# Optimization experiments

Hardware: AMD Instinct MI355X
Metric: run time of the kernel (lower is better)

Reference implementation:

```python
import jax, jax.numpy as jnp
import numpy as np

DIM = 2048
H = 16
HD = 128
S = 2640          # frame_seq_len(22*40=880) * num_frame_per_block(3)
CACHE = 5280      # 6 cached frames
MAXPOS = 8192
EPS = 1e-6


def rmsnorm(x, g, eps=EPS):
    return x * jax.lax.rsqrt(jnp.mean(x * x, axis=-1, keepdims=True) + eps) * g


def apply_rope_interleaved(x, cos, sin):
    # x: [s, H, HD]; cos/sin: [s, HD//2]; is_neox=False -> adjacent pairs
    x1 = x[..., 0::2]
    x2 = x[..., 1::2]
    c = cos[:, None, :]
    s_ = sin[:, None, :]
    o1 = x1 * c - x2 * s_
    o2 = x2 * c + x1 * s_
    return jnp.stack([o1, o2], axis=-1).reshape(x.shape)


def setup_inputs() -> dict:
    key = jax.random.key(0)
    ks = jax.random.split(key, 10)
    w_scale = DIM ** -0.5
    x = jax.random.normal(ks[0], (1, S, DIM), dtype=jnp.float32)
    # cos_sin_cache: [max_pos, HD] = [cos(HD//2) | sin(HD//2)], real rope values
    inv_freq = 1.0 / (10000.0 ** (np.arange(0, HD, 2, dtype=np.float32) / HD))
    t = np.arange(MAXPOS, dtype=np.float32)
    ang = np.outer(t, inv_freq)  # [MAXPOS, HD//2]
    freqs = jnp.asarray(np.concatenate([np.cos(ang), np.sin(ang)], axis=1), dtype=jnp.float32)
    k_cache = jax.random.normal(ks[1], (CACHE, H, HD), dtype=jnp.float32)
    v_cache = jax.random.normal(ks[2], (CACHE, H, HD), dtype=jnp.float32)
    Wq = jax.random.normal(ks[3], (DIM, DIM), dtype=jnp.float32) * w_scale
    Wk = jax.random.normal(ks[4], (DIM, DIM), dtype=jnp.float32) * w_scale
    Wv = jax.random.normal(ks[5], (DIM, DIM), dtype=jnp.float32) * w_scale
    Wo = jax.random.normal(ks[6], (DIM, DIM), dtype=jnp.float32) * w_scale
    bq = jnp.zeros((DIM,), jnp.float32)
    bk = jnp.zeros((DIM,), jnp.float32)
    bv = jnp.zeros((DIM,), jnp.float32)
    bo = jnp.zeros((DIM,), jnp.float32)
    gq = jnp.ones((DIM,), jnp.float32)
    gk = jnp.ones((DIM,), jnp.float32)
    return {"x": x, "freqs": freqs, "k_cache": k_cache, "v_cache": v_cache,
            "Wq": Wq, "bq": bq, "Wk": Wk, "bk": bk, "Wv": Wv, "bv": bv,
            "Wo": Wo, "bo": bo, "gq": gq, "gk": gk, "current_start": CACHE}


def reference(x, freqs, k_cache, v_cache, Wq, bq, Wk, bk, Wv, bv, Wo, bo, gq, gk, current_start):
    s = x.shape[1]
    xf = x[0]                                   # [s, DIM], B==1
    q = rmsnorm(xf @ Wq.T + bq, gq).reshape(s, H, HD)
    k = rmsnorm(xf @ Wk.T + bk, gk).reshape(s, H, HD)
    v = (xf @ Wv.T + bv).reshape(s, H, HD)
    # fused RoPE via cos_sin_cache lookup, interleaved (is_neox=False)
    positions = jnp.arange(s, dtype=jnp.int32) + current_start
    cs = freqs[positions]                       # [s, HD]
    cos, sin = cs[:, : HD // 2], cs[:, HD // 2:]
    rq = apply_rope_interleaved(q, cos, sin)
    rk = apply_rope_interleaved(k, cos, sin)
    # streaming attention: full access to cache, causal within incoming block
    k_all = jnp.concatenate([k_cache, rk], axis=0)  # [L, H, HD]
    v_all = jnp.concatenate([v_cache, v], axis=0)
    L = k_all.shape[0]
    scale = HD ** -0.5
    scores = jnp.einsum("qhd,khd->hqk", rq, k_all) * scale  # [H, s, L]
    kv_idx = jnp.arange(L)
    q_idx = jnp.arange(s)
    mask = (kv_idx[None, :] - (L - s)) <= q_idx[:, None]    # cache always visible
    scores = jnp.where(mask[None, :, :], scores, jnp.float32(-1e30))
    attn = jax.nn.softmax(scores, axis=-1)
    out = jnp.einsum("hqk,khd->qhd", attn, v_all).reshape(s, DIM)
    y = out @ Wo.T + bo
    return y[None]                              # [1, s, DIM]
```

## Files before the change

kernel.cpp:

```cpp
#include <hip/hip_runtime.h>

#define DIMN 2048
#define NH 16
#define HDIM 128

typedef __attribute__((ext_vector_type(4))) float f32x4;
typedef __attribute__((ext_vector_type(8))) __bf16 bfx8;
typedef __attribute__((ext_vector_type(8))) unsigned short u16x8;
typedef __attribute__((ext_vector_type(4))) unsigned short u16x4;

__device__ __forceinline__ unsigned short f2bf(float f){
  unsigned u = __builtin_bit_cast(unsigned, f);
  u += 0x7fffu + ((u >> 16) & 1u);
  return (unsigned short)(u >> 16);
}
__device__ __forceinline__ float bf2f(unsigned short h){
  unsigned u = (unsigned)h << 16;
  return __builtin_bit_cast(float, u);
}

__device__ __forceinline__ void gl_lds16(const void* g, void* l){
  __builtin_amdgcn_global_load_lds((const __attribute__((address_space(1))) void*)g,
                                   (__attribute__((address_space(3))) void*)l, 16, 0, 0);
}

#define MFMA16(a,b,c) __builtin_amdgcn_mfma_f32_16x16x32_bf16((a),(b),(c),0,0,0)

__global__ __launch_bounds__(256) void cast_bf16_kernel(const float* __restrict__ in,
                                                        unsigned short* __restrict__ out, int n8){
  int i = blockIdx.x*256 + threadIdx.x;
  if (i >= n8) return;
  const float4* p = (const float4*)(in + (size_t)i*8);
  float4 a = p[0], b = p[1];
  u16x8 o;
  o[0]=f2bf(a.x); o[1]=f2bf(a.y); o[2]=f2bf(a.z); o[3]=f2bf(a.w);
  o[4]=f2bf(b.x); o[5]=f2bf(b.y); o[6]=f2bf(b.z); o[7]=f2bf(b.w);
  *(u16x8*)(out + (size_t)i*8) = o;
}

__global__ __launch_bounds__(256) void kcache_kernel(const float* __restrict__ kc,
                                                     unsigned short* __restrict__ kb,
                                                     int R, int L_){
  const int gid = blockIdx.x*256 + threadIdx.x;
  if (gid >= R*256) return;
  const size_t idx = (size_t)gid * 8;
  const int k   = (int)(idx >> 11);
  const int rem = (int)(idx & 2047);
  const int hh  = rem >> 7, d = rem & 127;
  const float4* p = (const float4*)(kc + idx);
  float4 a = p[0], b = p[1];
  u16x8 o;
  o[0]=f2bf(a.x); o[1]=f2bf(a.y); o[2]=f2bf(a.z); o[3]=f2bf(a.w);
  o[4]=f2bf(b.x); o[5]=f2bf(b.y); o[6]=f2bf(b.z); o[7]=f2bf(b.w);
  *(u16x8*)(kb + (size_t)hh*L_*HDIM + (size_t)k*HDIM + d) = o;
}

__global__ __launch_bounds__(256) void vtrans_kernel(const float* __restrict__ src,
                                                     unsigned short* __restrict__ vt,
                                                     int R, int koff, int L_){
  __shared__ __align__(16) unsigned short tile[32][72];
  const int kb0 = blockIdx.x * 64, db0 = blockIdx.y * 32, hh = blockIdx.z;
  const int t = threadIdx.x;
  const int kk = t >> 2, dd = (t & 3) * 8;
  const int k = kb0 + kk;
  if (k < R){
    const float* p = src + (size_t)k*DIMN + hh*HDIM + db0 + dd;
    float4 a = ((const float4*)p)[0], b = ((const float4*)p)[1];
    tile[dd+0][kk] = f2bf(a.x); tile[dd+1][kk] = f2bf(a.y);
    tile[dd+2][kk] = f2bf(a.z); tile[dd+3][kk] = f2bf(a.w);
    tile[dd+4][kk] = f2bf(b.x); tile[dd+5][kk] = f2bf(b.y);
    tile[dd+6][kk] = f2bf(b.z); tile[dd+7][kk] = f2bf(b.w);
  }
  __syncthreads();
  const int d = t >> 3, k0 = (t & 7) * 8;
  unsigned short* dst = vt + (size_t)hh*HDIM*L_ + (size_t)(db0+d)*L_ + koff + kb0 + k0;
  if (kb0 + k0 + 8 <= R){
    *(u16x8*)dst = *(const u16x8*)&tile[d][k0];
  } else {
    #pragma unroll
    for (int e=0;e<8;++e) if (kb0 + k0 + e < R) dst[e] = tile[d][k0+e];
  }
}

__global__ __launch_bounds__(256) void vtrans_bf16_kernel(const unsigned short* __restrict__ src,
    unsigned short* __restrict__ vt, int R, int koff, int L_){
  __shared__ __align__(16) unsigned short tile[32][72];
  const int kb0 = blockIdx.x * 64, db0 = blockIdx.y * 32, hh = blockIdx.z;
  const int t = threadIdx.x;
  const int kk = t >> 2, dd = (t & 3) * 8;
  const int k = kb0 + kk;
  if (k < R){
    u16x8 a = *(const u16x8*)(src + (size_t)k*DIMN + hh*HDIM + db0 + dd);
    #pragma unroll
    for (int e=0;e<8;++e) tile[dd+e][kk] = a[e];
  }
  __syncthreads();
  const int d = t >> 3, k0 = (t & 7) * 8;
  unsigned short* dst = vt + (size_t)hh*HDIM*L_ + (size_t)(db0+d)*L_ + koff + kb0 + k0;
  if (kb0 + k0 + 8 <= R){
    *(u16x8*)dst = *(const u16x8*)&tile[d][k0];
  } else {
    #pragma unroll
    for (int e=0;e<8;++e) if (kb0 + k0 + e < R) dst[e] = tile[d][k0+e];
  }
}

__global__ __launch_bounds__(256) void norm_rope_kernel(const unsigned short* __restrict__ lin,
    const float* __restrict__ g, const float* __restrict__ freqs, const int* __restrict__ cur,
    unsigned short* __restrict__ out, int S_, size_t head_stride, int row_off){
  const int q = blockIdx.x, t = threadIdx.x;
  u16x8 v = *(const u16x8*)(lin + (size_t)q*DIMN + t*8);
  float x[8];
  #pragma unroll
  for (int e=0;e<8;++e) x[e] = bf2f(v[e]);
  float ss = 0.f;
  #pragma unroll
  for (int e=0;e<8;++e) ss += x[e]*x[e];
  for (int m=1;m<64;m<<=1) ss += __shfl_xor(ss, m);
  __shared__ float red[4];
  if ((t & 63) == 0) red[t>>6] = ss;
  __syncthreads();
  const float tot = red[0]+red[1]+red[2]+red[3];
  const float rstd = rsqrtf(tot * (1.0f/2048.0f) + 1e-6f);
  const int n0 = t*8;
  float xr[8];
  #pragma unroll
  for (int e=0;e<8;++e) xr[e] = x[e] * rstd * g[n0+e];
  const int pos = cur[0] + q;
  const int hh = n0 >> 7, d0 = n0 & 127;
  const float* fr = freqs + (size_t)pos * HDIM;
  float o[8];
  #pragma unroll
  for (int p=0;p<4;++p){
    const int j = (d0>>1) + p;
    const float c = fr[j], s = fr[64+j];
    o[2*p]   = xr[2*p]*c - xr[2*p+1]*s;
    o[2*p+1] = xr[2*p+1]*c + xr[2*p]*s;
  }
  u16x8 ov;
  #pragma unroll
  for (int e=0;e<8;++e) ov[e] = f2bf(o[e]);
  *(u16x8*)(out + (size_t)hh*head_stride + (size_t)(q+row_off)*HDIM + d0) = ov;
}

__global__ __launch_bounds__(256,2) void gemm_bt(const unsigned short* __restrict__ A,
    const unsigned short* __restrict__ B, const float* __restrict__ bias,
    float* __restrict__ C, int M, int N, int K){
  __shared__ __align__(16) unsigned short As[128*64];
  __shared__ __align__(16) unsigned short Bs[128*64];
  const int t = threadIdx.x;
  const int w = t >> 6, lane = t & 63, lh = lane >> 4, ll = lane & 15;
  const int wr = w >> 1, wc = w & 1;
  const int m0 = blockIdx.y * 128, n0 = blockIdx.x * 128;
  const int srow = t >> 3;
  const int scb  = (t & 7) * 16;
  const int swc  = (scb ^ ((srow & 7) << 4)) >> 1;
  int arow[4]; size_t brow[4];
  #pragma unroll
  for (int c=0;c<4;++c){
    int r = m0 + c*32 + srow; if (r >= M) r = M-1;
    arow[c] = r;
    brow[c] = (size_t)(n0 + c*32 + srow);
  }
  const int xsw = (ll & 7) << 4;
  f32x4 acc[4][4] = {};
  const int nk = K >> 6;
  for (int kt = 0; kt < nk; ++kt){
    const int k0 = kt << 6;
    #pragma unroll
    for (int c=0;c<4;++c){
      gl_lds16(A + (size_t)arow[c]*K + k0 + swc, (char*)As + c*4096 + w*1024);
      gl_lds16(B + brow[c]*K       + k0 + swc, (char*)Bs + c*4096 + w*1024);
    }
    asm volatile("s_waitcnt vmcnt(0)" ::: "memory");
    __syncthreads();
    #pragma unroll
    for (int kk=0;kk<2;++kk){
      const int cb = kk*64 + lh*16;
      bfx8 a[4], b[4];
      #pragma unroll
      for (int i=0;i<4;++i)
        a[i] = *(const bfx8*)((const char*)As + (wr*64 + i*16 + ll)*128 + (cb ^ xsw));
      #pragma unroll
      for (int j=0;j<4;++j)
        b[j] = *(const bfx8*)((const char*)Bs + (wc*64 + j*16 + ll)*128 + (cb ^ xsw));
      #pragma unroll
      for (int i=0;i<4;++i)
        #pragma unroll
        for (int j=0;j<4;++j)
          acc[i][j] = MFMA16(a[i], b[j], acc[i][j]);
    }
    __syncthreads();
  }
  #pragma unroll
  for (int i=0;i<4;++i){
    #pragma unroll
    for (int j=0;j<4;++j){
      const int col = n0 + wc*64 + j*16 + ll;
      const float bb = bias[col];
      #pragma unroll
      for (int r=0;r<4;++r){
        const int row = m0 + wr*64 + i*16 + lh*4 + r;
        if (row < M) C[(size_t)row*N + col] = acc[i][j][r] + bb;
      }
    }
  }
}

__global__ __launch_bounds__(256,2) void gemm_qkv(const unsigned short* __restrict__ A,
    const unsigned short* __restrict__ B0, const unsigned short* __restrict__ B1,
    const unsigned short* __restrict__ B2, const float* __restrict__ g0,
    const float* __restrict__ g1, const float* __restrict__ g2,
    unsigned short* __restrict__ C0, unsigned short* __restrict__ C1,
    unsigned short* __restrict__ C2, int M, int N, int K){
  const int zz = blockIdx.z;
  const unsigned short* B = (zz==0) ? B0 : (zz==1) ? B1 : B2;
  const float* bias       = (zz==0) ? g0 : (zz==1) ? g1 : g2;
  unsigned short* C       = (zz==0) ? C0 : (zz==1) ? C1 : C2;
  __shared__ __align__(16) unsigned short As[128*64];
  __shared__ __align__(16) unsigned short Bs[128*64];
  const int t = threadIdx.x;
  const int w = t >> 6, lane = t & 63, lh = lane >> 4, ll = lane & 15;
  const int wr = w >> 1, wc = w & 1;
  const int m0 = blockIdx.y * 128, n0 = blockIdx.x * 128;
  const int srow = t >> 3;
  const int scb  = (t & 7) * 16;
  const int swc  = (scb ^ ((srow & 7) << 4)) >> 1;
  int arow[4]; size_t brow[4];
  #pragma unroll
  for (int c=0;c<4;++c){
    int r = m0 + c*32 + srow; if (r >= M) r = M-1;
    arow[c] = r;
    brow[c] = (size_t)(n0 + c*32 + srow);
  }
  const int xsw = (ll & 7) << 4;
  f32x4 acc[4][4] = {};
  const int nk = K >> 6;
  for (int kt = 0; kt < nk; ++kt){
    const int k0 = kt << 6;
    #pragma unroll
    for (int c=0;c<4;++c){
      gl_lds16(A + (size_t)arow[c]*K + k0 + swc, (char*)As + c*4096 + w*1024);
      gl_lds16(B + brow[c]*K       + k0 + swc, (char*)Bs + c*4096 + w*1024);
    }
    asm volatile("s_waitcnt vmcnt(0)" ::: "memory");
    __syncthreads();
    #pragma unroll
    for (int kk=0;kk<2;++kk){
      const int cb = kk*64 + lh*16;
      bfx8 a[4], b[4];
      #pragma unroll
      for (int i=0;i<4;++i)
        a[i] = *(const bfx8*)((const char*)As + (wr*64 + i*16 + ll)*128 + (cb ^ xsw));
      #pragma unroll
      for (int j=0;j<4;++j)
        b[j] = *(const bfx8*)((const char*)Bs + (wc*64 + j*16 + ll)*128 + (cb ^ xsw));
      #pragma unroll
      for (int i=0;i<4;++i)
        #pragma unroll
        for (int j=0;j<4;++j)
          acc[i][j] = MFMA16(a[i], b[j], acc[i][j]);
    }
    __syncthreads();
  }
  #pragma unroll
  for (int i=0;i<4;++i){
    #pragma unroll
    for (int j=0;j<4;++j){
      const int col = n0 + wc*64 + j*16 + ll;
      const float bb = bias[col];
      #pragma unroll
      for (int r=0;r<4;++r){
        const int row = m0 + wr*64 + i*16 + lh*4 + r;
        if (row < M) C[(size_t)row*N + col] = f2bf(acc[i][j][r] + bb);
      }
    }
  }
}

__global__ __launch_bounds__(256,2) void attn_kernel(const unsigned short* __restrict__ Q,
    const unsigned short* __restrict__ K, const unsigned short* __restrict__ VT,
    unsigned short* __restrict__ O, float* __restrict__ pacc, float* __restrict__ pml,
    int S_, int L_, int CLn, int nsplit){
  __shared__ __align__(16) unsigned short Ks[2][64*128];
  __shared__ __align__(16) unsigned short Vs[2][128*64];
  __shared__ __align__(16) unsigned short Ps[4][32*64];
  const int hh = blockIdx.y;
  const int q0 = blockIdx.x * 128;
  const int z  = blockIdx.z;
  const int t = threadIdx.x, w = t >> 6, lane = t & 63, lh = lane >> 4, ll = lane & 15;
  const int xsw = (ll & 7) << 4;
  char* Pw = (char*)Ps[w];
  const unsigned short* Qh = Q  + (size_t)hh*S_*HDIM;
  const unsigned short* Kh = K  + (size_t)hh*L_*HDIM;
  const unsigned short* Vh = VT + (size_t)hh*HDIM*L_;
  bfx8 qf[2][4];
  #pragma unroll
  for (int i=0;i<2;++i){
    int qr = q0 + w*32 + i*16 + ll; if (qr >= S_) qr = S_ - 1;
    #pragma unroll
    for (int kk=0;kk<4;++kk)
      qf[i][kk] = *(const bfx8*)(Qh + (size_t)qr*HDIM + kk*32 + lh*8);
  }
  f32x4 acc[2][8] = {};
  float m_st[2], l_st[2];
  m_st[0] = m_st[1] = -1e20f;
  l_st[0] = l_st[1] = 0.f;
  const int wrow0 = q0 + w*32;
  int qlast = q0 + 127; if (qlast >= S_) qlast = S_ - 1;
  const int kend = CLn + qlast + 1;
  const int nt = (kend + 63) >> 6;
  const int tps = (nt + nsplit - 1) / nsplit;
  const int t0 = z * tps;
  int t1 = t0 + tps; if (t1 > nt) t1 = nt;
  const float scale = 0.08838834764831845f;
  const int ksrow = t >> 4, kchunk = t & 15;
  const int vsrow = t >> 3, vchunk = t & 7;
  const int myq[2] = { wrow0 + ll, wrow0 + 16 + ll };

  u16x8 kreg[4], vreg[4];
  auto load_tile = [&](int ktile){
    const int kv0 = ktile << 6;
    #pragma unroll
    for (int c=0;c<4;++c){
      int krow = kv0 + c*16 + ksrow; if (krow >= L_) krow = L_ - 1;
      kreg[c] = *(const u16x8*)(Kh + (size_t)krow*HDIM + kchunk*8);
      int vcol = kv0 + vchunk*8; if (vcol > L_ - 8) vcol = L_ - 8;
      vreg[c] = *(const u16x8*)(Vh + (size_t)(c*32 + vsrow)*L_ + vcol);
    }
  };
  auto stage_write = [&](int b){
    #pragma unroll
    for (int c=0;c<4;++c){
      *(u16x8*)((char*)Ks[b] + (c*16 + ksrow)*256 + ((kchunk*16) ^ ((ksrow & 7) << 4))) = kreg[c];
      *(u16x8*)((char*)Vs[b] + (c*32 + vsrow)*128 + ((vchunk*16) ^ ((vsrow & 7) << 4))) = vreg[c];
    }
  };
  if (t0 < t1){
    load_tile(t0);
    stage_write(0);
    if (t0 + 1 < t1) load_tile(t0 + 1);
  }
  int cur = 0;
  for (int kt = t0; kt < t1; ++kt){
    const int kv0 = kt << 6;
    __syncthreads();
    const char* Kc = (const char*)Ks[cur];
    const char* Vc = (const char*)Vs[cur];
    f32x4 sc[2][4] = {};
    #pragma unroll
    for (int kk=0;kk<4;++kk){
      const int cb = kk*64 + lh*16;
      #pragma unroll
      for (int j=0;j<4;++j){
        bfx8 kf = *(const bfx8*)(Kc + (j*16 + ll)*256 + (cb ^ xsw));
        sc[0][j] = MFMA16(kf, qf[0][kk], sc[0][j]);
        sc[1][j] = MFMA16(kf, qf[1][kk], sc[1][j]);
      }
    }
    if (kt + 1 < t1){
      stage_write(cur ^ 1);
      if (kt + 2 < t1) load_tile(kt + 2);
    }
    const bool needmask = (kv0 + 63 > CLn + wrow0);
    if (needmask){
      #pragma unroll
      for (int i=0;i<2;++i){
        const int lim = CLn + myq[i];
        #pragma unroll
        for (int j=0;j<4;++j)
          #pragma unroll
          for (int r=0;r<4;++r){
            const int key = kv0 + j*16 + lh*4 + r;
            sc[i][j][r] = (key > lim) ? -1e30f : sc[i][j][r]*scale;
          }
      }
    } else {
      #pragma unroll
      for (int i=0;i<2;++i)
        #pragma unroll
        for (int j=0;j<4;++j)
          #pragma unroll
          for (int r=0;r<4;++r) sc[i][j][r] *= scale;
    }
    float m_t[2];
    #pragma unroll
    for (int i=0;i<2;++i){
      float mt = sc[i][0][0];
      #pragma unroll
      for (int j=0;j<4;++j)
        #pragma unroll
        for (int r=0;r<4;++r) mt = fmaxf(mt, sc[i][j][r]);
      mt = fmaxf(mt, __shfl_xor(mt, 16));
      mt = fmaxf(mt, __shfl_xor(mt, 32));
      m_t[i] = fmaxf(mt, -1e20f);
    }
    const float mdiff = fmaxf(m_t[0] - m_st[0], m_t[1] - m_st[1]);
    if (!__all(mdiff <= 8.0f)){
      float corr[2];
      #pragma unroll
      for (int i=0;i<2;++i){
        const float mn = fmaxf(m_st[i], m_t[i]);
        corr[i] = __expf(m_st[i] - mn);
        m_st[i] = mn;
        l_st[i] *= corr[i];
      }
      #pragma unroll
      for (int i=0;i<2;++i)
        #pragma unroll
        for (int r=0;r<4;++r){
          const float ca = __shfl(corr[i], lh*4 + r);
          #pragma unroll
          for (int jn=0;jn<8;++jn) acc[i][jn][r] *= ca;
        }
    }
    #pragma unroll
    for (int i=0;i<2;++i){
      float rs = 0.f;
      #pragma unroll
      for (int j=0;j<4;++j)
        #pragma unroll
        for (int r=0;r<4;++r){
          const float pv = __expf(sc[i][j][r] - m_st[i]);
          sc[i][j][r] = pv;
          rs += pv;
        }
      rs += __shfl_xor(rs, 16);
      rs += __shfl_xor(rs, 32);
      l_st[i] += rs;
    }
    #pragma unroll
    for (int i=0;i<2;++i)
      #pragma unroll
      for (int j=0;j<4;++j){
        u16x4 pk;
        #pragma unroll
        for (int r=0;r<4;++r) pk[r] = f2bf(sc[i][j][r]);
        *(u16x4*)(Pw + (i*16 + ll)*128 + ((j*32 + lh*8) ^ xsw)) = pk;
      }
    #pragma unroll
    for (int kk=0;kk<2;++kk){
      const int cb = kk*64 + lh*16;
      bfx8 af0 = *(const bfx8*)(Pw + (ll)*128      + (cb ^ xsw));
      bfx8 af1 = *(const bfx8*)(Pw + (16 + ll)*128 + (cb ^ xsw));
      #pragma unroll
      for (int jn=0;jn<8;++jn){
        bfx8 vf = *(const bfx8*)(Vc + (jn*16 + ll)*128 + (cb ^ xsw));
        acc[0][jn] = MFMA16(af0, vf, acc[0][jn]);
        acc[1][jn] = MFMA16(af1, vf, acc[1][jn]);
      }
    }
    cur ^= 1;
  }
  if (nsplit == 1){
    #pragma unroll
    for (int i=0;i<2;++i){
      const float linv = 1.0f / l_st[i];
      #pragma unroll
      for (int r=0;r<4;++r){
        const float inv = __shfl(linv, lh*4 + r);
        const int qr = wrow0 + i*16 + lh*4 + r;
        if (qr < S_){
          #pragma unroll
          for (int jn=0;jn<8;++jn)
            O[(size_t)qr*DIMN + hh*HDIM + jn*16 + ll] = f2bf(acc[i][jn][r]*inv);
        }
      }
    }
  } else {
    #pragma unroll
    for (int i=0;i<2;++i){
      #pragma unroll
      for (int r=0;r<4;++r){
        const int qr = wrow0 + i*16 + lh*4 + r;
        if (qr < S_){
          const size_t rid = ((size_t)z*NH + hh)*S_ + qr;
          float* dst = pacc + rid*128;
          #pragma unroll
          for (int jn=0;jn<8;++jn) dst[jn*16 + ll] = acc[i][jn][r];
        }
      }
      if (lane < 16){
        const int qr2 = myq[i];
        if (qr2 < S_){
          const size_t rid2 = ((size_t)z*NH + hh)*S_ + qr2;
          pml[rid2*2]   = m_st[i];
          pml[rid2*2+1] = l_st[i];
        }
      }
    }
  }
}

__global__ __launch_bounds__(256) void combine_kernel(const float* __restrict__ pacc,
    const float* __restrict__ pml, unsigned short* __restrict__ ob, int S_, int nsplit){
  const int t = threadIdx.x;
  const int rid = blockIdx.x*2 + (t >> 7);
  if (rid >= S_*NH) return;
  const int d = t & 127;
  const int hh = rid / S_;
  const int q  = rid - hh*S_;
  float M = -1e20f;
  for (int s=0; s<nsplit; ++s)
    M = fmaxf(M, pml[((size_t)s*NH*S_ + rid)*2]);
  float lt = 0.f, o = 0.f;
  for (int s=0; s<nsplit; ++s){
    const float m = pml[((size_t)s*NH*S_ + rid)*2];
    const float l = pml[((size_t)s*NH*S_ + rid)*2 + 1];
    const float wgt = __expf(m - M);
    lt += l * wgt;
    o  += pacc[((size_t)s*NH*S_ + rid)*128 + d] * wgt;
  }
  if (lt == 0.f) lt = 1.f;
  ob[(size_t)q*DIMN + hh*HDIM + d] = f2bf(o / lt);
}

extern "C" void kernel_launch(void* const* d_in, const int* in_sizes, int n_in,
                              void* d_out, int out_size, void* d_ws, size_t ws_size,
                              hipStream_t stream){
  const float* x       = (const float*)d_in[0];
  const float* freqs   = (const float*)d_in[1];
  const float* k_cache = (const float*)d_in[2];
  const float* v_cache = (const float*)d_in[3];
  const float* Wq = (const float*)d_in[4];
  const float* bq = (const float*)d_in[5];
  const float* Wk = (const float*)d_in[6];
  const float* bk = (const float*)d_in[7];
  const float* Wv = (const float*)d_in[8];
  const float* bv = (const float*)d_in[9];
  const float* Wo = (const float*)d_in[10];
  const float* bo = (const float*)d_in[11];
  const float* gq = (const float*)d_in[12];
  const float* gk = (const float*)d_in[13];
  const int*   cur = (const int*)d_in[14];

  const int S = in_sizes[0] / DIMN;
  const int CACHE_ = in_sizes[2] / DIMN;
  const int L = CACHE_ + S;
  const int CLn = L - S;

  auto al = [](size_t n){ return (n + 255) & ~(size_t)255; };
  char* base = (char*)d_ws;
  size_t off = 0;
  auto take = [&](size_t n){ char* r = base + off; off += al(n); return r; };
  unsigned short* xb  = (unsigned short*)take((size_t)S*DIMN*2);
  unsigned short* Wob = (unsigned short*)take((size_t)DIMN*DIMN*2);
  unsigned short* qb  = (unsigned short*)take((size_t)NH*S*HDIM*2);
  unsigned short* kb  = (unsigned short*)take((size_t)NH*L*HDIM*2);
  unsigned short* vtb = (unsigned short*)take((size_t)NH*HDIM*L*2);
  unsigned short* ob  = (unsigned short*)take((size_t)S*DIMN*2);
  const size_t ubase = off;
  const size_t l_sz = al((size_t)S*DIMN*2);
  const size_t w_sz = al((size_t)DIMN*DIMN*2);
  unsigned short* lin0 = (unsigned short*)(base + ubase);
  unsigned short* lin1 = (unsigned short*)(base + ubase + l_sz);
  unsigned short* lin2 = (unsigned short*)(base + ubase + 2*l_sz);
  unsigned short* Wqb  = (unsigned short*)(base + ubase + 3*l_sz);
  unsigned short* Wkb  = (unsigned short*)(base + ubase + 3*l_sz + w_sz);
  unsigned short* Wvb  = (unsigned short*)(base + ubase + 3*l_sz + 2*w_sz);
  const size_t trans_sz = 3*l_sz + 3*w_sz;
  auto pool_sz = [&](int ns){
    return al((size_t)ns*NH*S*HDIM*4) + al((size_t)ns*NH*S*2*4);
  };
  int nsplit = 1;
  if (ubase + (trans_sz > pool_sz(4) ? trans_sz : pool_sz(4)) <= ws_size) nsplit = 4;
  else if (ubase + (trans_sz > pool_sz(2) ? trans_sz : pool_sz(2)) <= ws_size) nsplit = 2;
  if (ubase + trans_sz > ws_size) return;
  float* pacc = (float*)(base + ubase);
  float* pml  = (float*)(base + ubase + al((size_t)nsplit*NH*S*HDIM*4));

  const int wn8 = DIMN*DIMN/8;
  cast_bf16_kernel<<<(S*DIMN/8+255)/256, 256, 0, stream>>>(x,  xb,  S*DIMN/8);
  cast_bf16_kernel<<<(wn8+255)/256, 256, 0, stream>>>(Wq, Wqb, wn8);
  cast_bf16_kernel<<<(wn8+255)/256, 256, 0, stream>>>(Wk, Wkb, wn8);
  cast_bf16_kernel<<<(wn8+255)/256, 256, 0, stream>>>(Wv, Wvb, wn8);
  cast_bf16_kernel<<<(wn8+255)/256, 256, 0, stream>>>(Wo, Wob, wn8);
  kcache_kernel<<<CACHE_, 256, 0, stream>>>(k_cache, kb, CACHE_, L);
  vtrans_kernel<<<dim3((CACHE_+63)/64, 4, NH), 256, 0, stream>>>(v_cache, vtb, CACHE_, 0, L);

  const int mb = (S+127)/128;
  gemm_qkv<<<dim3(DIMN/128, mb, 3), 256, 0, stream>>>(xb, Wqb, Wkb, Wvb, bq, bk, bv,
                                                      lin0, lin1, lin2, S, DIMN, DIMN);
  norm_rope_kernel<<<S, 256, 0, stream>>>(lin0, gq, freqs, cur, qb, S, (size_t)S*HDIM, 0);
  norm_rope_kernel<<<S, 256, 0, stream>>>(lin1, gk, freqs, cur, kb, S, (size_t)L*HDIM, CACHE_);
  vtrans_bf16_kernel<<<dim3((S+63)/64, 4, NH), 256, 0, stream>>>(lin2, vtb, S, CACHE_, L);

  attn_kernel<<<dim3((S+127)/128, NH, nsplit), 256, 0, stream>>>(qb, kb, vtb, ob,
                                                                 pacc, pml, S, L, CLn, nsplit);
  if (nsplit > 1)
    combine_kernel<<<(S*NH+1)/2, 256, 0, stream>>>(pacc, pml, ob, S, nsplit);
  gemm_bt<<<dim3(DIMN/128, mb), 256, 0, stream>>>(ob, Wob, bo, (float*)d_out, S, DIMN, DIMN);
}
```

Measured before the change: 504.5 us.

## Fold softmax scale and log2e into Q, use exp2, packed bf16 cvt, swizzle grid

The softmax scale times log2(e) is folded into Q during the norm/RoPE pass, so the attention kernel no longer multiplies every score and can use exp2f instead of __expf. The lazy-rescale threshold is adjusted to the log2 domain. The P tile is converted with the v_cvt_pk_bf16_f32 instruction instead of manual rounding. The attention grid is flattened to 1D with an XCD-aware block-id swizzle to improve K/V cache locality. Q is rounded to bf16 after scaling, which adds a small precision difference.

After: 514.0 us. About the same (+1.9%).

```diff
diff --git a/kernel.cpp b/kernel.cpp
--- a/kernel.cpp
+++ b/kernel.cpp
@@ -7,7 +7,7 @@
 typedef __attribute__((ext_vector_type(4))) float f32x4;
 typedef __attribute__((ext_vector_type(8))) __bf16 bfx8;
 typedef __attribute__((ext_vector_type(8))) unsigned short u16x8;
-typedef __attribute__((ext_vector_type(4))) unsigned short u16x4;
+typedef __attribute__((ext_vector_type(2))) unsigned int u32x2;
 
 __device__ __forceinline__ unsigned short f2bf(float f){
   unsigned u = __builtin_bit_cast(unsigned, f);
@@ -17,6 +17,11 @@
 __device__ __forceinline__ float bf2f(unsigned short h){
   unsigned u = (unsigned)h << 16;
   return __builtin_bit_cast(float, u);
+}
+__device__ __forceinline__ unsigned cvt_pk_bf16(float lo, float hi){
+  unsigned r;
+  asm("v_cvt_pk_bf16_f32 %0, %1, %2" : "=v"(r) : "v"(lo), "v"(hi));
+  return r;
 }
 
 __device__ __forceinline__ void gl_lds16(const void* g, void* l){
@@ -107,7 +112,7 @@
 
 __global__ __launch_bounds__(256) void norm_rope_kernel(const unsigned short* __restrict__ lin,
     const float* __restrict__ g, const float* __restrict__ freqs, const int* __restrict__ cur,
-    unsigned short* __restrict__ out, int S_, size_t head_stride, int row_off){
+    unsigned short* __restrict__ out, int S_, size_t head_stride, int row_off, float oscale){
   const int q = blockIdx.x, t = threadIdx.x;
   u16x8 v = *(const u16x8*)(lin + (size_t)q*DIMN + t*8);
   float x[8];
@@ -139,7 +144,7 @@
   }
   u16x8 ov;
   #pragma unroll
-  for (int e=0;e<8;++e) ov[e] = f2bf(o[e]);
+  for (int e=0;e<8;++e) ov[e] = f2bf(o[e]*oscale);
   *(u16x8*)(out + (size_t)hh*head_stride + (size_t)(q+row_off)*HDIM + d0) = ov;
 }
 
@@ -281,13 +286,17 @@
 __global__ __launch_bounds__(256,2) void attn_kernel(const unsigned short* __restrict__ Q,
     const unsigned short* __restrict__ K, const unsigned short* __restrict__ VT,
     unsigned short* __restrict__ O, float* __restrict__ pacc, float* __restrict__ pml,
-    int S_, int L_, int CLn, int nsplit){
+    int S_, int L_, int CLn, int nx, int nsplit){
   __shared__ __align__(16) unsigned short Ks[2][64*128];
   __shared__ __align__(16) unsigned short Vs[2][128*64];
   __shared__ __align__(16) unsigned short Ps[4][32*64];
-  const int hh = blockIdx.y;
-  const int q0 = blockIdx.x * 128;
-  const int z  = blockIdx.z;
+  const int nwg = gridDim.x;
+  const int swzid = (blockIdx.x & 7)*(nwg >> 3) + (blockIdx.x >> 3);
+  const int xq = swzid % nx;
+  const int rest = swzid / nx;
+  const int hh = rest % NH;
+  const int z  = rest / NH;
+  const int q0 = xq * 128;
   const int t = threadIdx.x, w = t >> 6, lane = t & 63, lh = lane >> 4, ll = lane & 15;
   const int xsw = (ll & 7) << 4;
   char* Pw = (char*)Ps[w];
@@ -313,7 +322,6 @@
   const int tps = (nt + nsplit - 1) / nsplit;
   const int t0 = z * tps;
   int t1 = t0 + tps; if (t1 > nt) t1 = nt;
-  const float scale = 0.08838834764831845f;
   const int ksrow = t >> 4, kchunk = t & 15;
   const int vsrow = t >> 3, vchunk = t & 7;
   const int myq[2] = { wrow0 + ll, wrow0 + 16 + ll };
@@ -372,16 +380,9 @@
           #pragma unroll
           for (int r=0;r<4;++r){
             const int key = kv0 + j*16 + lh*4 + r;
-            sc[i][j][r] = (key > lim) ? -1e30f : sc[i][j][r]*scale;
+            if (key > lim) sc[i][j][r] = -1e30f;
           }
       }
-    } else {
-      #pragma unroll
-      for (int i=0;i<2;++i)
-        #pragma unroll
-        for (int j=0;j<4;++j)
-          #pragma unroll
-          for (int r=0;r<4;++r) sc[i][j][r] *= scale;
     }
     float m_t[2];
     #pragma unroll
@@ -396,12 +397,12 @@
       m_t[i] = fmaxf(mt, -1e20f);
     }
     const float mdiff = fmaxf(m_t[0] - m_st[0], m_t[1] - m_st[1]);
-    if (!__all(mdiff <= 8.0f)){
+    if (!__all(mdiff <= 11.54f)){
       float corr[2];
       #pragma unroll
       for (int i=0;i<2;++i){
         const float mn = fmaxf(m_st[i], m_t[i]);
-        corr[i] = __expf(m_st[i] - mn);
+        corr[i] = exp2f(m_st[i] - mn);
         m_st[i] = mn;
         l_st[i] *= corr[i];
       }
@@ -421,7 +422,7 @@
       for (int j=0;j<4;++j)
         #pragma unroll
         for (int r=0;r<4;++r){
-          const float pv = __expf(sc[i][j][r] - m_st[i]);
+          const float pv = exp2f(sc[i][j][r] - m_st[i]);
           sc[i][j][r] = pv;
           rs += pv;
         }
@@ -433,10 +434,10 @@
     for (int i=0;i<2;++i)
       #pragma unroll
       for (int j=0;j<4;++j){
-        u16x4 pk;
-        #pragma unroll
-        for (int r=0;r<4;++r) pk[r] = f2bf(sc[i][j][r]);
-        *(u16x4*)(Pw + (i*16 + ll)*128 + ((j*32 + lh*8) ^ xsw)) = pk;
+        u32x2 pk;
+        pk[0] = cvt_pk_bf16(sc[i][j][0], sc[i][j][1]);
+        pk[1] = cvt_pk_bf16(sc[i][j][2], sc[i][j][3]);
+        *(u32x2*)(Pw + (i*16 + ll)*128 + ((j*32 + lh*8) ^ xsw)) = pk;
       }
     #pragma unroll
     for (int kk=0;kk<2;++kk){
@@ -507,7 +508,7 @@
   for (int s=0; s<nsplit; ++s){
     const float m = pml[((size_t)s*NH*S_ + rid)*2];
     const float l = pml[((size_t)s*NH*S_ + rid)*2 + 1];
-    const float wgt = __expf(m - M);
+    const float wgt = exp2f(m - M);
     lt += l * wgt;
     o  += pacc[((size_t)s*NH*S_ + rid)*128 + d] * wgt;
   }
@@ -581,12 +582,14 @@
   const int mb = (S+127)/128;
   gemm_qkv<<<dim3(DIMN/128, mb, 3), 256, 0, stream>>>(xb, Wqb, Wkb, Wvb, bq, bk, bv,
                                                       lin0, lin1, lin2, S, DIMN, DIMN);
-  norm_rope_kernel<<<S, 256, 0, stream>>>(lin0, gq, freqs, cur, qb, S, (size_t)S*HDIM, 0);
-  norm_rope_kernel<<<S, 256, 0, stream>>>(lin1, gk, freqs, cur, kb, S, (size_t)L*HDIM, CACHE_);
+  const float qsc = 0.08838834764831845f * 1.4426950408889634f;
+  norm_rope_kernel<<<S, 256, 0, stream>>>(lin0, gq, freqs, cur, qb, S, (size_t)S*HDIM, 0, qsc);
+  norm_rope_kernel<<<S, 256, 0, stream>>>(lin1, gk, freqs, cur, kb, S, (size_t)L*HDIM, CACHE_, 1.0f);
   vtrans_bf16_kernel<<<dim3((S+63)/64, 4, NH), 256, 0, stream>>>(lin2, vtb, S, CACHE_, L);
 
-  attn_kernel<<<dim3((S+127)/128, NH, nsplit), 256, 0, stream>>>(qb, kb, vtb, ob,
-                                                                 pacc, pml, S, L, CLn, nsplit);
+  const int nx = (S+127)/128;
+  attn_kernel<<<nx*NH*nsplit, 256, 0, stream>>>(qb, kb, vtb, ob,
+                                                pacc, pml, S, L, CLn, nx, nsplit);
   if (nsplit > 1)
     combine_kernel<<<(S*NH+1)/2, 256, 0, stream>>>(pacc, pml, ob, S, nsplit);
   gemm_bt<<<dim3(DIMN/128, mb), 256, 0, stream>>>(ob, Wob, bo, (float*)d_out, S, DIMN, DIMN);
```
